# Optimization experiments

Measured on AMD Instinct MI355X. Metric: run time of the kernel, lower is better.

The kernel has to match this reference:

```python
import jax, jax.numpy as jnp
import numpy as np

R_MAX = 5.0
N_BESSEL = 8
AVG_NEIGH = 32.0
SQRT3 = 3.0 ** 0.5
SQRT2 = 2.0 ** 0.5


def _sph_harm(vec):
    # real spherical harmonics up to l=1, e3nn 'component' normalization:
    # Y0 = 1, Y1 = sqrt(3) * unit_vector
    r = jnp.linalg.norm(vec, axis=-1, keepdims=True)  # [E,1]
    u = vec / (r + 1e-9)
    y0 = jnp.ones_like(r)
    return jnp.concatenate([y0, SQRT3 * u], axis=-1), r[..., 0]  # [E,4],[E]


def _radial(lengths):
    # Bessel radial basis * polynomial cutoff envelope (p=6), as in MACE
    u = lengths / R_MAX
    n = jnp.arange(1, N_BESSEL + 1, dtype=lengths.dtype)
    bess = (2.0 / R_MAX) ** 0.5 * jnp.sin(n * jnp.pi * u[:, None]) / (lengths[:, None] + 1e-9)
    p = 6.0
    env = 1.0 - (p + 1.0) * (p + 2.0) / 2.0 * u ** 6 + p * (p + 2.0) * u ** 7 - p * (p + 1.0) / 2.0 * u ** 8
    env = jnp.where(u < 1.0, env, 0.0)
    return bess * env[:, None]  # [E, N_BESSEL]


def _forward(node_attrs, atom_pos, shifts, W_embed, Wup_s, Wup_v, RW1, RW2, RW3,
             Wout_s, Wout_v, Wsc_s, Wsc_v, P0, P1, Wprod_s, Wprod_v, edge_index):
    N = node_attrs.shape[0]
    sender, receiver = edge_index[0], edge_index[1]
    vec = atom_pos[receiver] - atom_pos[sender] + shifts          # [E,3]
    edge_attrs, lengths = _sph_harm(vec)                          # [E,4],[E]
    edge_feats = _radial(lengths)                                 # [E,8]
    Y0 = edge_attrs[:, 0:1]                                       # [E,1]
    Y1 = edge_attrs[:, 1:4]                                       # [E,3]

    s = node_attrs @ W_embed                                      # node embedding -> [N,C] scalars
    C = s.shape[1]
    v = jnp.zeros((N, C, 3), s.dtype)                             # l=1 features start at zero

    desc = []
    n_layers = Wup_s.shape[0]
    for i in range(n_layers):
        # linear_up: per-l channel mixing
        s_up = s @ Wup_s[i]
        v_up = jnp.einsum('nci,cd->ndi', v, Wup_v[i])
        # radial MLP -> per-edge tensor-product path weights [E,5C]
        h = jax.nn.silu(edge_feats @ RW1[i])
        h = jax.nn.silu(h @ RW2[i])
        w = h @ RW3[i]
        w00, w110, w011, w101, w111 = jnp.split(w, 5, axis=-1)    # each [E,C]
        # gather sender features, CG tensor product with edge SH (paths for lmax=1)
        sj = s_up[sender]                                         # [E,C]
        vj = v_up[sender]                                         # [E,C,3]
        m0 = w00 * sj * Y0 + w110 * jnp.einsum('eci,ei->ec', vj, Y1) / SQRT3
        m1 = (w011[:, :, None] * sj[:, :, None] * Y1[:, None, :]
              + w101[:, :, None] * vj * Y0[:, :, None]
              + w111[:, :, None] * jnp.cross(vj, Y1[:, None, :]) / SQRT2)
        # scatter-reduce messages into receiver nodes
        agg0 = jax.ops.segment_sum(m0, receiver, num_segments=N) / AVG_NEIGH
        agg1 = jax.ops.segment_sum(m1, receiver, num_segments=N) / AVG_NEIGH
        ms = agg0 @ Wout_s[i]
        mv = jnp.einsum('nci,cd->ndi', agg1, Wout_v[i])
        # element-dependent skip connection (node_attrs x node_feats FCTP)
        sc_s = jnp.einsum('nc,nz,zcd->nd', s, node_attrs, Wsc_s[i])
        sc_v = jnp.einsum('nci,nz,zcd->ndi', v, node_attrs, Wsc_v[i])
        # equivariant product basis (symmetric contraction, element-dependent weights)
        p = jnp.einsum('nz,zck->nck', node_attrs, P0[i])          # [N,C,3]
        q = jnp.einsum('nz,zck->nck', node_attrs, P1[i])          # [N,C,2]
        prod_s = p[..., 0] * ms + p[..., 1] * ms * ms + p[..., 2] * jnp.sum(mv * mv, axis=-1)
        prod_v = q[..., 0:1] * mv + q[..., 1:2] * ms[:, :, None] * mv
        s = prod_s @ Wprod_s[i] + sc_s
        v = jnp.einsum('nci,cd->ndi', prod_v, Wprod_v[i]) + sc_v
        # extract_scalar_irreps: first irrep block = l=0 channels
        desc.append(s)
    return jnp.concatenate(desc, axis=-1)                         # [N, n_layers*C]


def setup_inputs() -> dict:
    key = jax.random.key(0)
    ks = jax.random.split(key, 18)
    N, E, C, Z, L, H = 20000, 320000, 64, 10, 2, 64
    species = jax.random.randint(ks[0], (N,), 0, Z)
    node_attrs = jax.nn.one_hot(species, Z, dtype=jnp.float32)
    atom_pos = jax.random.uniform(ks[1], (N, 3), jnp.float32) * 5.0
    edge_index = jax.random.randint(ks[2], (2, E), 0, N)
    shifts = jnp.zeros((E, 3), jnp.float32)

    def w(k, shape, fan_in):
        return jax.random.normal(k, shape, jnp.float32) / np.sqrt(fan_in)

    return {
        'node_attrs': node_attrs,
        'atom_pos': atom_pos,
        'shifts': shifts,
        'W_embed': w(ks[3], (Z, C), Z),
        'Wup_s': w(ks[4], (L, C, C), C),
        'Wup_v': w(ks[5], (L, C, C), C),
        'RW1': w(ks[6], (L, N_BESSEL, H), N_BESSEL),
        'RW2': w(ks[7], (L, H, H), H),
        'RW3': w(ks[8], (L, H, 5 * C), H),
        'Wout_s': w(ks[9], (L, C, C), C),
        'Wout_v': w(ks[10], (L, C, C), C),
        'Wsc_s': w(ks[11], (L, Z, C, C), C),
        'Wsc_v': w(ks[12], (L, Z, C, C), C),
        'P0': w(ks[13], (L, Z, C, 3), 1),
        'P1': w(ks[14], (L, Z, C, 2), 1),
        'Wprod_s': w(ks[15], (L, C, C), C),
        'Wprod_v': w(ks[16], (L, C, C), C),
        'edge_index': edge_index,
    }


def reference(node_attrs, atom_pos, shifts, W_embed, Wup_s, Wup_v, RW1, RW2, RW3,
              Wout_s, Wout_v, Wsc_s, Wsc_v, P0, P1, Wprod_s, Wprod_v, edge_index):
    return _forward(node_attrs, atom_pos, shifts, W_embed, Wup_s, Wup_v, RW1, RW2, RW3,
                    Wout_s, Wout_v, Wsc_s, Wsc_v, P0, P1, Wprod_s, Wprod_v, edge_index)
```

## Files before the change

kernel.cpp:

```cpp
#include <hip/hip_runtime.h>
#include <hip/hip_bf16.h>
#include <hip/hip_fp16.h>

typedef _Float16 half8 __attribute__((ext_vector_type(8)));
typedef float floatx4 __attribute__((ext_vector_type(4)));

union F2H { float f; _Float16 h[2]; };

__device__ __forceinline__ float siluf(float x) {
    return x / (1.0f + __expf(-x));
}

__global__ void k_species(const float* __restrict__ attrs, int* __restrict__ species_o,
                          int* __restrict__ zcount, int N) {
    int n = blockIdx.x * 256 + threadIdx.x;
    if (n >= N) return;
    int z = 0;
    #pragma unroll
    for (int k = 1; k < 10; k++) if (attrs[n * 10 + k] > 0.5f) z = k;
    species_o[n] = z;
    atomicAdd(&zcount[z], 1);
}

__global__ void k_zscan(const int* __restrict__ zcount, int* __restrict__ zcur,
                        int* __restrict__ zstart) {
    if (threadIdx.x == 0) {
        int run = 0;
        for (int z = 0; z < 10; z++) {
            zstart[z] = run;
            zcur[z] = run;
            run += (zcount[z] + 15) & ~15;
        }
        zstart[10] = run;
    }
}

__global__ void k_zperm(const int* __restrict__ species_o, int* __restrict__ zcur,
                        int* __restrict__ perm_n, int* __restrict__ inv_n, int N) {
    int n = blockIdx.x * 256 + threadIdx.x;
    if (n >= N) return;
    int pos = atomicAdd(&zcur[species_o[n]], 1);
    perm_n[pos] = n;
    inv_n[n] = pos;
}

__global__ void k_padmark(const int* __restrict__ zstart, const int* __restrict__ zcur,
                          int* __restrict__ perm_n, int* __restrict__ deg,
                          int* __restrict__ species_s, int Npad) {
    int p = blockIdx.x * 256 + threadIdx.x;
    if (p >= Npad) return;
    deg[p] = 0;
    if (p >= zstart[10]) {
        perm_n[p] = -1;
        species_s[p] = 9;
        return;
    }
    int z = 9;
    #pragma unroll
    for (int q = 0; q < 10; q++) {
        if (p < zstart[q + 1]) { z = q; break; }
    }
    if (p >= zcur[z]) {
        perm_n[p] = -1;
        species_s[p] = z;
    }
}

__global__ void k_init(const int* __restrict__ perm_n, const int* __restrict__ species_o,
                       const float* __restrict__ Wemb, int* __restrict__ species_s,
                       int* __restrict__ origid, float* __restrict__ s,
                       float* __restrict__ v, int Npad) {
    int p = blockIdx.x * 4 + (threadIdx.x >> 6);
    if (p >= Npad) return;
    int lane = threadIdx.x & 63;
    int n = perm_n[p];
    if (n < 0) {
        if (lane == 0) origid[p] = -1;
        s[(size_t)p * 64 + lane] = 0.0f;
        v[(size_t)p * 192 + lane] = 0.0f;
        v[(size_t)p * 192 + 64 + lane] = 0.0f;
        v[(size_t)p * 192 + 128 + lane] = 0.0f;
        return;
    }
    int z = species_o[n];
    if (lane == 0) { species_s[p] = z; origid[p] = n; }
    s[(size_t)p * 64 + lane] = Wemb[z * 64 + lane];
    v[(size_t)p * 192 + lane] = 0.0f;
    v[(size_t)p * 192 + 64 + lane] = 0.0f;
    v[(size_t)p * 192 + 128 + lane] = 0.0f;
}

__global__ void k_hist(const int* __restrict__ ei, const int* __restrict__ inv_n,
                       int* __restrict__ deg, int E) {
    int e = blockIdx.x * 256 + threadIdx.x;
    if (e < E) atomicAdd(&deg[inv_n[ei[E + e]]], 1);
}

__global__ void k_scan(const int* __restrict__ deg, int* __restrict__ rowptr,
                       int* __restrict__ cursor, int N) {
    __shared__ int part[1024];
    int t = threadIdx.x;
    int chunk = (N + 1023) / 1024;
    int lo = t * chunk, hi = min(lo + chunk, N);
    int sum = 0;
    for (int i = lo; i < hi; i++) sum += deg[i];
    part[t] = sum;
    __syncthreads();
    for (int off = 1; off < 1024; off <<= 1) {
        int add = (t >= off) ? part[t - off] : 0;
        __syncthreads();
        part[t] += add;
        __syncthreads();
    }
    int run = (t > 0) ? part[t - 1] : 0;
    for (int i = lo; i < hi; i++) { rowptr[i] = run; cursor[i] = run; run += deg[i]; }
    if (t == 1023) rowptr[N] = part[1023];
}

__global__ void k_eperm(const int* __restrict__ ei, const int* __restrict__ inv_n,
                        int* __restrict__ cursor, int* __restrict__ perm, int E) {
    int e = blockIdx.x * 256 + threadIdx.x;
    if (e < E) {
        int r = inv_n[ei[E + e]];
        int pos = atomicAdd(&cursor[r], 1);
        perm[pos] = e;
    }
}

__global__ void k_geom(const int* __restrict__ ei, const int* __restrict__ perm,
                       const int* __restrict__ inv_n, const float* __restrict__ pos,
                       const float* __restrict__ shifts, float4* __restrict__ geo,
                       _Float16* __restrict__ efh, int* __restrict__ snd_s,
                       int* __restrict__ rcv_s, int E, int Epad, int padnode) {
    int j = blockIdx.x * 256 + threadIdx.x;
    if (j >= Epad) return;
    if (j >= E) {
        geo[j] = make_float4(0.0f, 0.0f, 0.0f, 0.0f);
        snd_s[j] = padnode;
        rcv_s[j] = padnode;
        half8 z8;
        #pragma unroll
        for (int k = 0; k < 8; k++) z8[k] = (_Float16)0.0f;
        *(half8*)(efh + (size_t)j * 8) = z8;
        return;
    }
    int e = perm[j];
    int snd = ei[e], rcv = ei[E + e];
    float dx = pos[rcv * 3 + 0] - pos[snd * 3 + 0] + shifts[e * 3 + 0];
    float dy = pos[rcv * 3 + 1] - pos[snd * 3 + 1] + shifts[e * 3 + 1];
    float dz = pos[rcv * 3 + 2] - pos[snd * 3 + 2] + shifts[e * 3 + 2];
    float r = sqrtf(dx * dx + dy * dy + dz * dz);
    float rin = 1.0f / (r + 1e-9f);
    const float SQ3 = 1.7320508075688772f;
    geo[j] = make_float4(SQ3 * dx * rin, SQ3 * dy * rin, SQ3 * dz * rin, 0.0f);
    snd_s[j] = inv_n[snd];
    rcv_s[j] = inv_n[rcv];
    float u = r * 0.2f;
    float env = 0.0f;
    if (u < 1.0f) {
        float u2 = u * u;
        float u6 = u2 * u2 * u2;
        env = 1.0f - 28.0f * u6 + 48.0f * u6 * u - 21.0f * u6 * u2;
    }
    const float PIF = 3.14159265358979f;
    float x = PIF * u;
    float sp = __sinf(x), cp = __cosf(x);
    float coef = 0.6324555320336759f * rin * env;
    float sm1 = 0.0f, scur = sp, twoc = 2.0f * cp;
    half8 e8;
    #pragma unroll
    for (int k = 0; k < 8; k++) {
        e8[k] = (_Float16)(coef * scur);
        float nxt = twoc * scur - sm1;
        sm1 = scur; scur = nxt;
    }
    *(half8*)(efh + (size_t)j * 8) = e8;
}

__global__ void k_wprep(const float* __restrict__ RW1, const float* __restrict__ RW2,
                        const float* __restrict__ RW3, _Float16* __restrict__ B1f,
                        _Float16* __restrict__ B2f, _Float16* __restrict__ B3f) {
    int lane = threadIdx.x;
    int t = blockIdx.x;
    int layer = t / 52;
    int tt = t % 52;
    int quad = lane >> 4, colx = lane & 15;
    if (tt < 4) {
        int nt = tt;
        const float* W = RW1 + (size_t)layer * 512;
        _Float16* dst = B1f + (size_t)layer * 2048 + ((size_t)nt * 64 + lane) * 8;
        #pragma unroll
        for (int j = 0; j < 8; j++) {
            int k = quad * 8 + j, n = nt * 16 + colx;
            dst[j] = (k < 8) ? (_Float16)W[k * 64 + n] : (_Float16)0.0f;
        }
    } else if (tt < 12) {
        int u = tt - 4;
        int kt = u >> 2, nt = u & 3;
        const float* W = RW2 + (size_t)layer * 4096;
        _Float16* dst = B2f + (size_t)layer * 4096 + (((size_t)kt * 4 + nt) * 64 + lane) * 8;
        #pragma unroll
        for (int j = 0; j < 8; j++) {
            int k = kt * 32 + quad * 8 + j, n = nt * 16 + colx;
            dst[j] = (_Float16)W[k * 64 + n];
        }
    } else {
        int u = tt - 12;
        int kt = u / 20, nt = u % 20;
        const float* W = RW3 + (size_t)layer * 20480;
        _Float16* dst = B3f + (size_t)layer * 20480 + (((size_t)kt * 20 + nt) * 64 + lane) * 8;
        const float inv32 = 1.0f / 32.0f;
        const float is3 = 0.5773502691896258f;
        const float is2 = 0.7071067811865476f;
        #pragma unroll
        for (int j = 0; j < 8; j++) {
            int k = kt * 32 + quad * 8 + j, n = nt * 16 + colx;
            int grp = n >> 6;
            float scale = inv32 * (grp == 1 ? is3 : (grp == 4 ? is2 : 1.0f));
            dst[j] = (_Float16)(W[k * 320 + n] * scale);
        }
    }
}

__global__ void k_wprep_node(const float* __restrict__ Wup_s, const float* __restrict__ Wup_v,
                             const float* __restrict__ Wout_s, const float* __restrict__ Wout_v,
                             const float* __restrict__ Wprod_s, const float* __restrict__ Wprod_v,
                             const float* __restrict__ Wsc_s, const float* __restrict__ Wsc_v,
                             _Float16* __restrict__ Bmats) {
    int mid = blockIdx.x;
    int layer = mid / 26, m = mid % 26;
    const float* src;
    if (m == 0)      src = Wup_s  + (size_t)layer * 4096;
    else if (m == 1) src = Wup_v  + (size_t)layer * 4096;
    else if (m == 2) src = Wout_s + (size_t)layer * 4096;
    else if (m == 3) src = Wout_v + (size_t)layer * 4096;
    else if (m == 4) src = Wprod_s + (size_t)layer * 4096;
    else if (m == 5) src = Wprod_v + (size_t)layer * 4096;
    else if (m < 16) src = Wsc_s + (size_t)layer * 40960 + (size_t)(m - 6) * 4096;
    else             src = Wsc_v + (size_t)layer * 40960 + (size_t)(m - 16) * 4096;
    _Float16* dst = Bmats + (size_t)mid * 4096;
    int lane = threadIdx.x, quad = lane >> 4, colx = lane & 15;
    for (int t = 0; t < 8; t++) {
        int kt = t >> 2, nt = t & 3;
        #pragma unroll
        for (int j = 0; j < 8; j++) {
            int k = kt * 32 + quad * 8 + j, n = nt * 16 + colx;
            dst[(size_t)t * 512 + lane * 8 + j] = (_Float16)src[k * 64 + n];
        }
    }
}

__device__ __forceinline__ half8 loadA(const float* __restrict__ base) {
    half8 a;
    float4 f0 = ((const float4*)base)[0];
    float4 f1 = ((const float4*)base)[1];
    a[0]=(_Float16)f0.x; a[1]=(_Float16)f0.y; a[2]=(_Float16)f0.z; a[3]=(_Float16)f0.w;
    a[4]=(_Float16)f1.x; a[5]=(_Float16)f1.y; a[6]=(_Float16)f1.z; a[7]=(_Float16)f1.w;
    return a;
}

__global__ __launch_bounds__(256, 4)
void k_nodeA(const float* __restrict__ s, const float* __restrict__ v,
             const int* __restrict__ species,
             const _Float16* __restrict__ Bup_s, const _Float16* __restrict__ Bup_v,
             const _Float16* __restrict__ Bsc_s, const _Float16* __restrict__ Bsc_v,
             float2* __restrict__ packh, float2* __restrict__ scph,
             float* __restrict__ agg0, float* __restrict__ agg1, int Npad) {
    const int tid = threadIdx.x;
    const int lane = tid & 63, wave = tid >> 6;
    const int quad = lane >> 4, col = lane & 15;
    const int n0 = blockIdx.x * 64 + wave * 16;
    if (n0 >= Npad) return;

    half8 as[2], av0[2], av1[2], av2[2];
    int node = n0 + col;
    const float* sp = s + (size_t)node * 64;
    const float* vp = v + (size_t)node * 192;
    #pragma unroll
    for (int kt = 0; kt < 2; kt++) {
        int kb = kt * 32 + quad * 8;
        as[kt]  = loadA(sp + kb);
        av0[kt] = loadA(vp + kb);
        av1[kt] = loadA(vp + 64 + kb);
        av2[kt] = loadA(vp + 128 + kb);
    }

    const int z = species[n0];
    const _Float16* Bs = Bsc_s + (size_t)z * 4096;
    const _Float16* Bv = Bsc_v + (size_t)z * 4096;

    #pragma unroll
    for (int nt = 0; nt < 4; nt++) {
        floatx4 cs = {0,0,0,0}, c0 = {0,0,0,0}, c1 = {0,0,0,0}, c2 = {0,0,0,0};
        floatx4 ds = {0,0,0,0}, d0 = {0,0,0,0}, d1 = {0,0,0,0}, d2 = {0,0,0,0};
        #pragma unroll
        for (int kt = 0; kt < 2; kt++) {
            half8 bs = *(const half8*)(Bup_s + (((size_t)kt * 4 + nt) * 64 + lane) * 8);
            half8 bv = *(const half8*)(Bup_v + (((size_t)kt * 4 + nt) * 64 + lane) * 8);
            half8 es = *(const half8*)(Bs + (((size_t)kt * 4 + nt) * 64 + lane) * 8);
            half8 ev = *(const half8*)(Bv + (((size_t)kt * 4 + nt) * 64 + lane) * 8);
            cs = __builtin_amdgcn_mfma_f32_16x16x32_f16(as[kt],  bs, cs, 0, 0, 0);
            c0 = __builtin_amdgcn_mfma_f32_16x16x32_f16(av0[kt], bv, c0, 0, 0, 0);
            c1 = __builtin_amdgcn_mfma_f32_16x16x32_f16(av1[kt], bv, c1, 0, 0, 0);
            c2 = __builtin_amdgcn_mfma_f32_16x16x32_f16(av2[kt], bv, c2, 0, 0, 0);
            ds = __builtin_amdgcn_mfma_f32_16x16x32_f16(as[kt],  es, ds, 0, 0, 0);
            d0 = __builtin_amdgcn_mfma_f32_16x16x32_f16(av0[kt], ev, d0, 0, 0, 0);
            d1 = __builtin_amdgcn_mfma_f32_16x16x32_f16(av1[kt], ev, d1, 0, 0, 0);
            d2 = __builtin_amdgcn_mfma_f32_16x16x32_f16(av2[kt], ev, d2, 0, 0, 0);
        }
        int ch = nt * 16 + col;
        #pragma unroll
        for (int r = 0; r < 4; r++) {
            int n = n0 + quad * 4 + r;
            F2H u1, u2, w1, w2;
            u1.h[0] = (_Float16)cs[r]; u1.h[1] = (_Float16)c0[r];
            u2.h[0] = (_Float16)c1[r]; u2.h[1] = (_Float16)c2[r];
            w1.h[0] = (_Float16)ds[r]; w1.h[1] = (_Float16)d0[r];
            w2.h[0] = (_Float16)d1[r]; w2.h[1] = (_Float16)d2[r];
            packh[(size_t)n * 64 + ch] = make_float2(u1.f, u2.f);
            scph[(size_t)n * 64 + ch]  = make_float2(w1.f, w2.f);
            agg0[(size_t)n * 64 + ch] = 0.0f;
            agg1[(size_t)n * 192 + ch] = 0.0f;
            agg1[(size_t)n * 192 + 64 + ch] = 0.0f;
            agg1[(size_t)n * 192 + 128 + ch] = 0.0f;
        }
    }
}

#define ROWP 72
#define MROW 66
__global__ __launch_bounds__(256, 4)
void k_msg(const _Float16* __restrict__ efh, const float4* __restrict__ geo,
           const int* __restrict__ snd_s, const int* __restrict__ rcv_s,
           const float2* __restrict__ packh,
           const _Float16* __restrict__ B1f, const _Float16* __restrict__ B2f,
           const _Float16* __restrict__ B3f,
           float* __restrict__ agg0, float* __restrict__ agg1) {
    __shared__ float2 mt[64 * MROW];
    _Float16* a2 = (_Float16*)mt;
    _Float16* a3 = (_Float16*)mt + 4608;
    const int tid = threadIdx.x;
    const int lane = tid & 63;
    const int wave = tid >> 6;
    const int quad = lane >> 4;
    const int col = lane & 15;
    const int j0 = blockIdx.x * 64 + wave * 16;

    _Float16* a2w = a2 + wave * 16 * ROWP;
    _Float16* a3w = a3 + wave * 16 * ROWP;

    half8 aef = *(const half8*)(efh + (size_t)(j0 + col) * 8);
    {
        floatx4 c1[4];
        #pragma unroll
        for (int nt = 0; nt < 4; nt++) {
            c1[nt] = (floatx4){0.0f, 0.0f, 0.0f, 0.0f};
            half8 b = *(const half8*)(B1f + ((size_t)nt * 64 + lane) * 8);
            c1[nt] = __builtin_amdgcn_mfma_f32_16x16x32_f16(aef, b, c1[nt], 0, 0, 0);
        }
        #pragma unroll
        for (int nt = 0; nt < 4; nt++)
            #pragma unroll
            for (int r = 0; r < 4; r++)
                a2w[(quad * 4 + r) * ROWP + nt * 16 + col] = (_Float16)siluf(c1[nt][r]);
    }
    __syncthreads();

    {
        half8 af0 = *(const half8*)&a2w[col * ROWP + quad * 8];
        half8 af1 = *(const half8*)&a2w[col * ROWP + 32 + quad * 8];
        floatx4 c2[4];
        #pragma unroll
        for (int nt = 0; nt < 4; nt++) {
            c2[nt] = (floatx4){0.0f, 0.0f, 0.0f, 0.0f};
            half8 b0 = *(const half8*)(B2f + (((size_t)0 * 4 + nt) * 64 + lane) * 8);
            half8 b1 = *(const half8*)(B2f + (((size_t)1 * 4 + nt) * 64 + lane) * 8);
            c2[nt] = __builtin_amdgcn_mfma_f32_16x16x32_f16(af0, b0, c2[nt], 0, 0, 0);
            c2[nt] = __builtin_amdgcn_mfma_f32_16x16x32_f16(af1, b1, c2[nt], 0, 0, 0);
        }
        #pragma unroll
        for (int nt = 0; nt < 4; nt++)
            #pragma unroll
            for (int r = 0; r < 4; r++)
                a3w[(quad * 4 + r) * ROWP + nt * 16 + col] = (_Float16)siluf(c2[nt][r]);
    }
    __syncthreads();

    half8 a3f0 = *(const half8*)&a3w[col * ROWP + quad * 8];
    half8 a3f1 = *(const half8*)&a3w[col * ROWP + 32 + quad * 8];
    __syncthreads();

    int sndr[4];
    float4 gr[4];
    #pragma unroll
    for (int r = 0; r < 4; r++) {
        int jj = j0 + quad * 4 + r;
        sndr[r] = snd_s[jj];
        gr[r] = geo[jj];
    }

    for (int cb = 0; cb < 4; cb++) {
        floatx4 acc[5];
        #pragma unroll
        for (int q = 0; q < 5; q++) {
            acc[q] = (floatx4){0.0f, 0.0f, 0.0f, 0.0f};
            int nt = q * 4 + cb;
            half8 b0 = *(const half8*)(B3f + (((size_t)0 * 20 + nt) * 64 + lane) * 8);
            half8 b1 = *(const half8*)(B3f + (((size_t)1 * 20 + nt) * 64 + lane) * 8);
            acc[q] = __builtin_amdgcn_mfma_f32_16x16x32_f16(a3f0, b0, acc[q], 0, 0, 0);
            acc[q] = __builtin_amdgcn_mfma_f32_16x16x32_f16(a3f1, b1, acc[q], 0, 0, 0);
        }
        const int c = cb * 16 + col;
        #pragma unroll
        for (int r = 0; r < 4; r++) {
            int m = quad * 4 + r;
            float4 g = gr[r];
            float2 pp = packh[(size_t)sndr[r] * 64 + c];
            F2H u1, u2; u1.f = pp.x; u2.f = pp.y;
            float pvx = (float)u1.h[0], pvy = (float)u1.h[1];
            float pvz = (float)u2.h[0], pvw = (float)u2.h[1];
            float w00 = acc[0][r], w110 = acc[1][r], w011 = acc[2][r];
            float w101 = acc[3][r], w111 = acc[4][r];
            float dvy = pvy * g.x + pvz * g.y + pvw * g.z;
            float m0 = w00 * pvx + w110 * dvy;
            float cxv = pvz * g.z - pvw * g.y;
            float cyv = pvw * g.x - pvy * g.z;
            float czv = pvy * g.y - pvz * g.x;
            float wps = w011 * pvx;
            float m1x = wps * g.x + w101 * pvy + w111 * cxv;
            float m1y = wps * g.y + w101 * pvz + w111 * cyv;
            float m1z = wps * g.z + w101 * pvw + w111 * czv;
            F2H o1, o2;
            o1.h[0] = (_Float16)m0;  o1.h[1] = (_Float16)m1x;
            o2.h[0] = (_Float16)m1y; o2.h[1] = (_Float16)m1z;
            mt[(wave * 16 + m) * MROW + c] = make_float2(o1.f, o2.f);
        }
    }

    {
        const int c = lane;
        const int jb = j0;
        float a0 = 0.0f, a1 = 0.0f, a2v = 0.0f, a3v = 0.0f;
        int prev = -1;
        #pragma unroll 4
        for (int i = 0; i < 16; i++) {
            int rr = rcv_s[jb + i];
            float2 mv = mt[(wave * 16 + i) * MROW + c];
            F2H u1, u2; u1.f = mv.x; u2.f = mv.y;
            float m0 = (float)u1.h[0], m1 = (float)u1.h[1];
            float m2 = (float)u2.h[0], m3 = (float)u2.h[1];
            if (rr != prev) {
                if (prev >= 0) {
                    atomicAdd(&agg0[(size_t)prev * 64 + c], a0);
                    atomicAdd(&agg1[(size_t)prev * 192 + c], a1);
                    atomicAdd(&agg1[(size_t)prev * 192 + 64 + c], a2v);
                    atomicAdd(&agg1[(size_t)prev * 192 + 128 + c], a3v);
                }
                a0 = m0; a1 = m1; a2v = m2; a3v = m3;
                prev = rr;
            } else {
                a0 += m0; a1 += m1; a2v += m2; a3v += m3;
            }
        }
        if (prev >= 0) {
            atomicAdd(&agg0[(size_t)prev * 64 + c], a0);
            atomicAdd(&agg1[(size_t)prev * 192 + c], a1);
            atomicAdd(&agg1[(size_t)prev * 192 + 64 + c], a2v);
            atomicAdd(&agg1[(size_t)prev * 192 + 128 + c], a3v);
        }
    }
}

#define ROWPB 72
__global__ __launch_bounds__(256, 4)
void k_nodeB(const float* __restrict__ agg0, const float* __restrict__ agg1,
             const int* __restrict__ species, const int* __restrict__ origid,
             const _Float16* __restrict__ Bout_s, const _Float16* __restrict__ Bout_v,
             const _Float16* __restrict__ Bprod_s, const _Float16* __restrict__ Bprod_v,
             const float* __restrict__ P0l, const float* __restrict__ P1l,
             const float2* __restrict__ scph, float* __restrict__ s,
             float* __restrict__ v, float* __restrict__ out,
             int Npad, int layer, int Ltot) {
    __shared__ _Float16 lds[4 * 4 * 16 * ROWPB];
    const int tid = threadIdx.x;
    const int lane = tid & 63, wave = tid >> 6;
    const int quad = lane >> 4, col = lane & 15;
    const int n0 = blockIdx.x * 64 + wave * 16;
    if (n0 >= Npad) return;
    _Float16* lw = lds + wave * 4 * 16 * ROWPB;

    const int z = species[n0];
    {
        half8 as[2], av0[2], av1[2], av2[2];
        int node = n0 + col;
        const float* ap = agg0 + (size_t)node * 64;
        const float* vp = agg1 + (size_t)node * 192;
        #pragma unroll
        for (int kt = 0; kt < 2; kt++) {
            int kb = kt * 32 + quad * 8;
            as[kt]  = loadA(ap + kb);
            av0[kt] = loadA(vp + kb);
            av1[kt] = loadA(vp + 64 + kb);
            av2[kt] = loadA(vp + 128 + kb);
        }
        #pragma unroll
        for (int nt = 0; nt < 4; nt++) {
            floatx4 cs = {0,0,0,0}, c0 = {0,0,0,0}, c1 = {0,0,0,0}, c2 = {0,0,0,0};
            #pragma unroll
            for (int kt = 0; kt < 2; kt++) {
                half8 bs = *(const half8*)(Bout_s + (((size_t)kt * 4 + nt) * 64 + lane) * 8);
                half8 bv = *(const half8*)(Bout_v + (((size_t)kt * 4 + nt) * 64 + lane) * 8);
                cs = __builtin_amdgcn_mfma_f32_16x16x32_f16(as[kt],  bs, cs, 0, 0, 0);
                c0 = __builtin_amdgcn_mfma_f32_16x16x32_f16(av0[kt], bv, c0, 0, 0, 0);
                c1 = __builtin_amdgcn_mfma_f32_16x16x32_f16(av1[kt], bv, c1, 0, 0, 0);
                c2 = __builtin_amdgcn_mfma_f32_16x16x32_f16(av2[kt], bv, c2, 0, 0, 0);
            }
            int ch = nt * 16 + col;
            const float* p = P0l + ((size_t)z * 64 + ch) * 3;
            const float* q = P1l + ((size_t)z * 64 + ch) * 2;
            float p0 = p[0], p1 = p[1], p2 = p[2];
            float q0 = q[0], q1 = q[1];
            #pragma unroll
            for (int r = 0; r < 4; r++) {
                int nl = quad * 4 + r;
                float msv = cs[r];
                float m0 = c0[r], m1 = c1[r], m2 = c2[r];
                float ps = p0 * msv + p1 * msv * msv + p2 * (m0 * m0 + m1 * m1 + m2 * m2);
                float qq = q0 + q1 * msv;
                lw[0 * 16 * ROWPB + nl * ROWPB + ch] = (_Float16)ps;
                lw[1 * 16 * ROWPB + nl * ROWPB + ch] = (_Float16)(qq * m0);
                lw[2 * 16 * ROWPB + nl * ROWPB + ch] = (_Float16)(qq * m1);
                lw[3 * 16 * ROWPB + nl * ROWPB + ch] = (_Float16)(qq * m2);
            }
        }
    }
    __syncthreads();
    {
        half8 as[2], av0[2], av1[2], av2[2];
        #pragma unroll
        for (int kt = 0; kt < 2; kt++) {
            int kb = kt * 32 + quad * 8;
            as[kt]  = *(const half8*)&lw[0 * 16 * ROWPB + col * ROWPB + kb];
            av0[kt] = *(const half8*)&lw[1 * 16 * ROWPB + col * ROWPB + kb];
            av1[kt] = *(const half8*)&lw[2 * 16 * ROWPB + col * ROWPB + kb];
            av2[kt] = *(const half8*)&lw[3 * 16 * ROWPB + col * ROWPB + kb];
        }
        int og[4];
        #pragma unroll
        for (int r = 0; r < 4; r++) og[r] = origid[n0 + quad * 4 + r];
        #pragma unroll
        for (int nt = 0; nt < 4; nt++) {
            floatx4 cs = {0,0,0,0}, c0 = {0,0,0,0}, c1 = {0,0,0,0}, c2 = {0,0,0,0};
            #pragma unroll
            for (int kt = 0; kt < 2; kt++) {
                half8 bs = *(const half8*)(Bprod_s + (((size_t)kt * 4 + nt) * 64 + lane) * 8);
                half8 bv = *(const half8*)(Bprod_v + (((size_t)kt * 4 + nt) * 64 + lane) * 8);
                cs = __builtin_amdgcn_mfma_f32_16x16x32_f16(as[kt],  bs, cs, 0, 0, 0);
                c0 = __builtin_amdgcn_mfma_f32_16x16x32_f16(av0[kt], bv, c0, 0, 0, 0);
                c1 = __builtin_amdgcn_mfma_f32_16x16x32_f16(av1[kt], bv, c1, 0, 0, 0);
                c2 = __builtin_amdgcn_mfma_f32_16x16x32_f16(av2[kt], bv, c2, 0, 0, 0);
            }
            int ch = nt * 16 + col;
            #pragma unroll
            for (int r = 0; r < 4; r++) {
                int n = n0 + quad * 4 + r;
                float2 scv = scph[(size_t)n * 64 + ch];
                F2H u1, u2; u1.f = scv.x; u2.f = scv.y;
                float sval = cs[r] + (float)u1.h[0];
                s[(size_t)n * 64 + ch] = sval;
                v[(size_t)n * 192 + ch] = c0[r] + (float)u1.h[1];
                v[(size_t)n * 192 + 64 + ch] = c1[r] + (float)u2.h[0];
                v[(size_t)n * 192 + 128 + ch] = c2[r] + (float)u2.h[1];
                if (og[r] >= 0)
                    out[(size_t)og[r] * (Ltot * 64) + layer * 64 + ch] = sval;
            }
        }
    }
}

extern "C" void kernel_launch(void* const* d_in, const int* in_sizes, int n_in,
                              void* d_out, int out_size, void* d_ws, size_t ws_size,
                              hipStream_t stream) {
    const float* node_attrs = (const float*)d_in[0];
    const float* atom_pos   = (const float*)d_in[1];
    const float* shifts     = (const float*)d_in[2];
    const float* W_embed    = (const float*)d_in[3];
    const float* Wup_s      = (const float*)d_in[4];
    const float* Wup_v      = (const float*)d_in[5];
    const float* RW1        = (const float*)d_in[6];
    const float* RW2        = (const float*)d_in[7];
    const float* RW3        = (const float*)d_in[8];
    const float* Wout_s     = (const float*)d_in[9];
    const float* Wout_v     = (const float*)d_in[10];
    const float* Wsc_s      = (const float*)d_in[11];
    const float* Wsc_v      = (const float*)d_in[12];
    const float* P0         = (const float*)d_in[13];
    const float* P1         = (const float*)d_in[14];
    const float* Wprod_s    = (const float*)d_in[15];
    const float* Wprod_v    = (const float*)d_in[16];
    const int*   ei         = (const int*)d_in[17];

    const int N = in_sizes[0] / 10;
    const int E = in_sizes[17] / 2;
    const int L = in_sizes[4] / 4096;
    const int Npad = ((N + 160) + 63) / 64 * 64;
    const int Epad = (E + 63) / 64 * 64;
    float* out = (float*)d_out;

    char* wsb = (char*)d_ws;
    size_t off = 0;
    auto alloci = [&](size_t n) {
        int* p = (int*)(wsb + off);
        off = (off + n * 4 + 255) / 256 * 256;
        return p;
    };
    auto allocf = [&](size_t n) {
        float* p = (float*)(wsb + off);
        off = (off + n * 4 + 255) / 256 * 256;
        return p;
    };
    auto alloch = [&](size_t n) {
        _Float16* p = (_Float16*)(wsb + off);
        off = (off + n * 2 + 255) / 256 * 256;
        return p;
    };
    int* species_o = alloci(N);
    int* species_s = alloci(Npad);
    int* zcount    = alloci(16);
    int* zcur      = alloci(16);
    int* zstart    = alloci(16);
    int* perm_n    = alloci(Npad);
    int* inv_n     = alloci(N);
    int* origid    = alloci(Npad);
    int* deg       = alloci(Npad);
    int* rowptr    = alloci(Npad + 1);
    int* cursor    = alloci(Npad);
    int* perm      = alloci(E);
    int* snd_s     = alloci(Epad);
    int* rcv_s     = alloci(Epad);
    float* s     = allocf((size_t)Npad * 64);
    float* v     = allocf((size_t)Npad * 192);
    float* agg0  = allocf((size_t)Npad * 64);
    float* agg1  = allocf((size_t)Npad * 192);
    float* geo   = allocf((size_t)Epad * 4);
    _Float16* efh = alloch((size_t)Epad * 8);
    float* packh = allocf((size_t)Npad * 128);
    float* scph  = allocf((size_t)Npad * 128);
    _Float16* B1f   = alloch((size_t)L * 2048);
    _Float16* B2f   = alloch((size_t)L * 4096);
    _Float16* B3f   = alloch((size_t)L * 20480);
    _Float16* Bmats = alloch((size_t)L * 26 * 4096);
    (void)n_in; (void)out_size; (void)ws_size;

    const int NT = Npad / 64;
    const int NB = (N + 255) / 256;
    const int NPB = (Npad + 255) / 256;
    const int EB = (E + 255) / 256;
    const int EPB = (Epad + 255) / 256;
    const int ET64 = Epad / 64;

    hipMemsetAsync(zcount, 0, 16 * sizeof(int), stream);
    k_species<<<NB, 256, 0, stream>>>(node_attrs, species_o, zcount, N);
    k_zscan<<<1, 64, 0, stream>>>(zcount, zcur, zstart);
    k_zperm<<<NB, 256, 0, stream>>>(species_o, zcur, perm_n, inv_n, N);
    k_padmark<<<NPB, 256, 0, stream>>>(zstart, zcur, perm_n, deg, species_s, Npad);
    k_init<<<(Npad + 3) / 4, 256, 0, stream>>>(perm_n, species_o, W_embed, species_s,
                                               origid, s, v, Npad);
    k_hist<<<EB, 256, 0, stream>>>(ei, inv_n, deg, E);
    k_scan<<<1, 1024, 0, stream>>>(deg, rowptr, cursor, Npad);
    k_eperm<<<EB, 256, 0, stream>>>(ei, inv_n, cursor, perm, E);
    k_geom<<<EPB, 256, 0, stream>>>(ei, perm, inv_n, atom_pos, shifts,
                                    (float4*)geo, efh, snd_s, rcv_s, E, Epad, Npad - 1);
    k_wprep<<<52 * L, 64, 0, stream>>>(RW1, RW2, RW3, B1f, B2f, B3f);
    k_wprep_node<<<26 * L, 64, 0, stream>>>(Wup_s, Wup_v, Wout_s, Wout_v,
                                            Wprod_s, Wprod_v, Wsc_s, Wsc_v, Bmats);

    for (int i = 0; i < L; i++) {
        const _Float16* Bl = Bmats + (size_t)i * 26 * 4096;
        k_nodeA<<<NT, 256, 0, stream>>>(s, v, species_s,
                                        Bl, Bl + 4096,
                                        Bl + 6 * 4096, Bl + 16 * 4096,
                                        (float2*)packh, (float2*)scph, agg0, agg1, Npad);
        k_msg<<<ET64, 256, 0, stream>>>(efh, (const float4*)geo, snd_s, rcv_s,
                                        (const float2*)packh,
                                        B1f + (size_t)i * 2048, B2f + (size_t)i * 4096,
                                        B3f + (size_t)i * 20480, agg0, agg1);
        k_nodeB<<<NT, 256, 0, stream>>>(agg0, agg1, species_s, origid,
                                        Bl + 2 * 4096, Bl + 3 * 4096,
                                        Bl + 4 * 4096, Bl + 5 * 4096,
                                        P0 + (size_t)i * 1920, P1 + (size_t)i * 1280,
                                        (const float2*)scph, s, v, out, Npad, i, L);
    }
}
```

Measured before the change: 612.6 us.

## Use single-wave blocks for node kernels and prefetch sender features in message kernel

The node kernels k_nodeA and k_nodeB now launch one 64-thread wave per block, each handling 16 nodes, with the LDS footprint in k_nodeB cut to match. This gives more blocks and finer scheduling granularity. In k_msg, the gathered sender features (packh) are loaded into registers at kernel start so the gather latency overlaps the radial MLP MFMAs. The shared-memory row stride shrinks and the occupancy hint rises to 5 blocks, at the cost of more register pressure from the 16 prefetched float2 values.

```diff
diff --git a/kernel.cpp b/kernel.cpp
--- a/kernel.cpp
+++ b/kernel.cpp
@@ -259,17 +259,16 @@
     return a;
 }
 
-__global__ __launch_bounds__(256, 4)
+__global__ __launch_bounds__(64, 4)
 void k_nodeA(const float* __restrict__ s, const float* __restrict__ v,
              const int* __restrict__ species,
              const _Float16* __restrict__ Bup_s, const _Float16* __restrict__ Bup_v,
              const _Float16* __restrict__ Bsc_s, const _Float16* __restrict__ Bsc_v,
              float2* __restrict__ packh, float2* __restrict__ scph,
              float* __restrict__ agg0, float* __restrict__ agg1, int Npad) {
-    const int tid = threadIdx.x;
-    const int lane = tid & 63, wave = tid >> 6;
+    const int lane = threadIdx.x & 63;
     const int quad = lane >> 4, col = lane & 15;
-    const int n0 = blockIdx.x * 64 + wave * 16;
+    const int n0 = blockIdx.x * 16;
     if (n0 >= Npad) return;
 
     half8 as[2], av0[2], av1[2], av2[2];
@@ -328,8 +327,8 @@
 }
 
 #define ROWP 72
-#define MROW 66
-__global__ __launch_bounds__(256, 4)
+#define MROW 64
+__global__ __launch_bounds__(256, 5)
 void k_msg(const _Float16* __restrict__ efh, const float4* __restrict__ geo,
            const int* __restrict__ snd_s, const int* __restrict__ rcv_s,
            const float2* __restrict__ packh,
@@ -349,6 +348,18 @@
     _Float16* a2w = a2 + wave * 16 * ROWP;
     _Float16* a3w = a3 + wave * 16 * ROWP;
 
+    float2 pp[4][4];
+    {
+        int sndr[4];
+        #pragma unroll
+        for (int r = 0; r < 4; r++) sndr[r] = snd_s[j0 + quad * 4 + r];
+        #pragma unroll
+        for (int cb = 0; cb < 4; cb++)
+            #pragma unroll
+            for (int r = 0; r < 4; r++)
+                pp[cb][r] = packh[(size_t)sndr[r] * 64 + cb * 16 + col];
+    }
+
     half8 aef = *(const half8*)(efh + (size_t)(j0 + col) * 8);
     {
         floatx4 c1[4];
@@ -390,14 +401,9 @@
     half8 a3f1 = *(const half8*)&a3w[col * ROWP + 32 + quad * 8];
     __syncthreads();
 
-    int sndr[4];
     float4 gr[4];
     #pragma unroll
-    for (int r = 0; r < 4; r++) {
-        int jj = j0 + quad * 4 + r;
-        sndr[r] = snd_s[jj];
-        gr[r] = geo[jj];
-    }
+    for (int r = 0; r < 4; r++) gr[r] = geo[j0 + quad * 4 + r];
 
     for (int cb = 0; cb < 4; cb++) {
         floatx4 acc[5];
@@ -415,8 +421,8 @@
         for (int r = 0; r < 4; r++) {
             int m = quad * 4 + r;
             float4 g = gr[r];
-            float2 pp = packh[(size_t)sndr[r] * 64 + c];
-            F2H u1, u2; u1.f = pp.x; u2.f = pp.y;
+            float2 ppv = pp[cb][r];
+            F2H u1, u2; u1.f = ppv.x; u2.f = ppv.y;
             float pvx = (float)u1.h[0], pvy = (float)u1.h[1];
             float pvz = (float)u2.h[0], pvw = (float)u2.h[1];
             float w00 = acc[0][r], w110 = acc[1][r], w011 = acc[2][r];
@@ -472,7 +478,7 @@
 }
 
 #define ROWPB 72
-__global__ __launch_bounds__(256, 4)
+__global__ __launch_bounds__(64, 4)
 void k_nodeB(const float* __restrict__ agg0, const float* __restrict__ agg1,
              const int* __restrict__ species, const int* __restrict__ origid,
              const _Float16* __restrict__ Bout_s, const _Float16* __restrict__ Bout_v,
@@ -481,13 +487,12 @@
              const float2* __restrict__ scph, float* __restrict__ s,
              float* __restrict__ v, float* __restrict__ out,
              int Npad, int layer, int Ltot) {
-    __shared__ _Float16 lds[4 * 4 * 16 * ROWPB];
-    const int tid = threadIdx.x;
-    const int lane = tid & 63, wave = tid >> 6;
+    __shared__ _Float16 lds[4 * 16 * ROWPB];
+    const int lane = threadIdx.x & 63;
     const int quad = lane >> 4, col = lane & 15;
-    const int n0 = blockIdx.x * 64 + wave * 16;
+    const int n0 = blockIdx.x * 16;
     if (n0 >= Npad) return;
-    _Float16* lw = lds + wave * 4 * 16 * ROWPB;
+    _Float16* lw = lds;
 
     const int z = species[n0];
     {
@@ -652,7 +657,7 @@
     _Float16* Bmats = alloch((size_t)L * 26 * 4096);
     (void)n_in; (void)out_size; (void)ws_size;
 
-    const int NT = Npad / 64;
+    const int NT16 = Npad / 16;
     const int NB = (N + 255) / 256;
     const int NPB = (Npad + 255) / 256;
     const int EB = (E + 255) / 256;
@@ -677,18 +682,18 @@
 
     for (int i = 0; i < L; i++) {
         const _Float16* Bl = Bmats + (size_t)i * 26 * 4096;
-        k_nodeA<<<NT, 256, 0, stream>>>(s, v, species_s,
-                                        Bl, Bl + 4096,
-                                        Bl + 6 * 4096, Bl + 16 * 4096,
-                                        (float2*)packh, (float2*)scph, agg0, agg1, Npad);
+        k_nodeA<<<NT16, 64, 0, stream>>>(s, v, species_s,
+                                         Bl, Bl + 4096,
+                                         Bl + 6 * 4096, Bl + 16 * 4096,
+                                         (float2*)packh, (float2*)scph, agg0, agg1, Npad);
         k_msg<<<ET64, 256, 0, stream>>>(efh, (const float4*)geo, snd_s, rcv_s,
                                         (const float2*)packh,
                                         B1f + (size_t)i * 2048, B2f + (size_t)i * 4096,
                                         B3f + (size_t)i * 20480, agg0, agg1);
-        k_nodeB<<<NT, 256, 0, stream>>>(agg0, agg1, species_s, origid,
-                                        Bl + 2 * 4096, Bl + 3 * 4096,
-                                        Bl + 4 * 4096, Bl + 5 * 4096,
-                                        P0 + (size_t)i * 1920, P1 + (size_t)i * 1280,
-                                        (const float2*)scph, s, v, out, Npad, i, L);
-    }
-}
+        k_nodeB<<<NT16, 64, 0, stream>>>(agg0, agg1, species_s, origid,
+                                         Bl + 2 * 4096, Bl + 3 * 4096,
+                                         Bl + 4 * 4096, Bl + 5 * 4096,
+                                         P0 + (size_t)i * 1920, P1 + (size_t)i * 1280,
+                                         (const float2*)scph, s, v, out, Npad, i, L);
+    }
+}
```

New measurement: 927.8 us. 1.51x slower.
